# Optimization experiments

Measured on AMD Instinct MI355X. Metric: run time of the kernel, lower is better.

## Reference

```python
import jax, jax.numpy as jnp
import numpy as np

B, S, D = 4, 2048, 2048
NH, NKV = 16, 4
HD = D // NH            # 128
DKV = NKV * HD          # 512
REP = NH // NKV         # 4
SCALE = HD ** -0.5
EPS = 1e-9


def setup_inputs() -> dict:
    key = jax.random.key(0)
    ks = jax.random.split(key, 9)
    s = 0.02
    return {
        "q": jax.random.normal(ks[0], (B, S, D), jnp.float32),
        "k": jax.random.normal(ks[1], (B, S, D), jnp.float32),
        "v": jax.random.normal(ks[2], (B, S, D), jnp.float32),
        "Wq": jax.random.normal(ks[3], (D, D), jnp.float32) * s,
        "bq": jnp.zeros((D,), jnp.float32),
        "Wk": jax.random.normal(ks[4], (D, DKV), jnp.float32) * s,
        "bk": jnp.zeros((DKV,), jnp.float32),
        "Wv": jax.random.normal(ks[5], (D, DKV), jnp.float32) * s,
        "bv": jnp.zeros((DKV,), jnp.float32),
    }


def reference(q, k, v, Wq, bq, Wk, bk, Wv, bv):
    # Dense projections (nn.Dense = x @ W + b)
    qh = q @ Wq + bq                      # (B, S, D)
    kh = k @ Wk + bk                      # (B, S, DKV)
    vh = v @ Wv + bv                      # (B, S, DKV)
    # Faithful to source: repeat along axis=-2 (the SEQUENCE axis)
    kh = jnp.repeat(kh, REP, axis=-2)     # (B, S*REP, DKV)
    vh = jnp.repeat(vh, REP, axis=-2)     # (B, S*REP, DKV)
    # flash_attention math: reshape to (B, S, NH, HD) -> (B, NH, S, HD)
    qh = qh.reshape(B, S, NH, HD).transpose(0, 2, 1, 3)
    kh = kh.reshape(B, S, NH, HD).transpose(0, 2, 1, 3)
    vh = vh.reshape(B, S, NH, HD).transpose(0, 2, 1, 3)
    attn = jnp.einsum("bhqd,bhkd->bhqk", qh, kh) * SCALE
    m = jnp.max(attn, axis=-1, keepdims=True)
    e = jnp.exp(attn - m)
    p = e / (jnp.sum(e, axis=-1, keepdims=True) + EPS)
    out = jnp.einsum("bhqk,bhkd->bhqd", p, vh)   # (B, NH, S, HD)
    return out.transpose(0, 2, 1, 3).reshape(B, S, D)
```

## Files before the change

kernel.cpp:

```cpp
#include <hip/hip_runtime.h>

#define B_    4
#define S_    2048
#define D_    2048
#define NH_   16
#define NKV_  4
#define HD_   128
#define DKV_  512
#define QSCALE_ ((float)(0.08838834764831845 * 1.4426950408889634))

typedef __attribute__((ext_vector_type(8))) short          bf16x8;
typedef __attribute__((ext_vector_type(8))) unsigned short us8;
typedef __attribute__((ext_vector_type(4))) unsigned short us4;
typedef __attribute__((ext_vector_type(4))) float          f32x4;

__device__ __forceinline__ unsigned short f2bf(float f) {
    union { float f; unsigned int u; } v; v.f = f;
    unsigned int u = v.u;
    u += 0x7fffu + ((u >> 16) & 1u);
    return (unsigned short)(u >> 16);
}

__device__ __forceinline__ unsigned int cvt_pk_bf16(float lo, float hi) {
    unsigned int r;
    asm volatile("v_cvt_pk_bf16_f32 %0, %1, %2" : "=v"(r) : "v"(lo), "v"(hi));
    return r;
}

__device__ __forceinline__ float vmax3(float a, float b, float c) {
    float r;
    asm("v_max3_f32 %0, %1, %2, %3" : "=v"(r) : "v"(a), "v"(b), "v"(c));
    return r;
}

#define GLOAD16(gp, lp) __builtin_amdgcn_global_load_lds(                      \
    (const __attribute__((address_space(1))) unsigned int*)(gp),              \
    (__attribute__((address_space(3))) unsigned int*)(lp), 16, 0, 0)

__device__ __forceinline__ void tr_body(
    const float* __restrict__ W, unsigned short* __restrict__ WT,
    int K, int N, int kb, int nb, float (*tile)[33])
{
    const int k0 = kb * 32, n0 = nb * 32;
    const int tx = threadIdx.x & 31, ty = threadIdx.x >> 5;
#pragma unroll
    for (int i = 0; i < 32; i += 8)
        tile[ty + i][tx] = W[(size_t)(k0 + ty + i) * N + n0 + tx];
    __syncthreads();
#pragma unroll
    for (int i = 0; i < 32; i += 8)
        WT[(size_t)(n0 + ty + i) * K + k0 + tx] = f2bf(tile[tx][ty + i]);
}

__global__ __launch_bounds__(256) void transpose_all(
    const float* __restrict__ Wq, const float* __restrict__ Wk,
    const float* __restrict__ Wv, unsigned short* __restrict__ WqT,
    unsigned short* __restrict__ WkT, unsigned short* __restrict__ WvT)
{
    __shared__ float tile[32][33];
    const int y = blockIdx.y;
    if (y < 64)       tr_body(Wq, WqT, D_, D_,   blockIdx.x, y,      tile);
    else if (y < 80)  tr_body(Wk, WkT, D_, DKV_, blockIdx.x, y - 64, tile);
    else              tr_body(Wv, WvT, D_, DKV_, blockIdx.x, y - 80, tile);
}

__device__ __forceinline__ void cvt_body(
    const float* __restrict__ src, unsigned short* __restrict__ dst, int n8)
{
    int i = blockIdx.x * blockDim.x + threadIdx.x;
    const int stride = gridDim.x * blockDim.x;
    const float4* p = (const float4*)src;
    us8* o8 = (us8*)dst;
    for (; i < n8; i += stride) {
        float4 a = p[2 * i], b = p[2 * i + 1];
        us8 o;
        o[0] = f2bf(a.x); o[1] = f2bf(a.y); o[2] = f2bf(a.z); o[3] = f2bf(a.w);
        o[4] = f2bf(b.x); o[5] = f2bf(b.y); o[6] = f2bf(b.z); o[7] = f2bf(b.w);
        o8[i] = o;
    }
}

__global__ __launch_bounds__(256) void cvt_bf16(
    const float* __restrict__ in, unsigned short* __restrict__ out, int n8)
{
    cvt_body(in, out, n8);
}

__global__ __launch_bounds__(256) void cvt_all(
    const float* __restrict__ q, const float* __restrict__ k,
    const float* __restrict__ v, unsigned short* __restrict__ xq,
    unsigned short* __restrict__ xk, unsigned short* __restrict__ xv)
{
    const int which = blockIdx.y;
    const float* src = which == 0 ? q : which == 1 ? k : v;
    unsigned short* dst = which == 0 ? xq : which == 1 ? xk : xv;
    cvt_body(src, dst, B_ * S_ * D_ / 8);
}

__device__ __forceinline__ void gemm_body(
    const unsigned short* __restrict__ A, const unsigned short* __restrict__ BT,
    const float* __restrict__ bias, unsigned short* __restrict__ C,
    int N, int nb, float scale, int vmode,
    unsigned short* As , unsigned short* Bs )
{
    const int K = D_;
    const int m0 = blockIdx.x * 128, n0 = nb * 128;
    const int t = threadIdx.x;
    const int w = t >> 6, l = t & 63, lr = l & 15, lg = l >> 4;
    const int wr = (w >> 1) * 64, wc = (w & 1) * 64;
    const int sr = t >> 2, sc = (t & 3) * 8;

    const unsigned short* aS = A + (size_t)(m0 + sr) * K + sc;
    const unsigned short* bS = BT + (size_t)(n0 + sr) * K + sc;

    auto stage = [&](int buf, int kt) {
        GLOAD16(aS + kt * 32,                    &As[buf * 4096 + t * 8]);
        GLOAD16(aS + (size_t)64 * K + kt * 32,   &As[buf * 4096 + 2048 + t * 8]);
        GLOAD16(bS + kt * 32,                    &Bs[buf * 4096 + t * 8]);
        GLOAD16(bS + (size_t)64 * K + kt * 32,   &Bs[buf * 4096 + 2048 + t * 8]);
    };

    f32x4 acc[4][4] = {};
    stage(0, 0);
    __syncthreads();

    const int nk = K / 32;
    int cur = 0;
    for (int kt = 0; kt < nk; ++kt) {
        if (kt + 1 < nk) stage(cur ^ 1, kt + 1);

        bf16x8 af[4], bfv[4];
#pragma unroll
        for (int i = 0; i < 4; ++i)
            af[i] = *(const bf16x8*)&As[cur * 4096 + (wr + i * 16 + lr) * 32 + lg * 8];
#pragma unroll
        for (int i = 0; i < 4; ++i)
            bfv[i] = *(const bf16x8*)&Bs[cur * 4096 + (wc + i * 16 + lr) * 32 + lg * 8];
#pragma unroll
        for (int i = 0; i < 4; ++i)
#pragma unroll
            for (int j = 0; j < 4; ++j)
                acc[i][j] = __builtin_amdgcn_mfma_f32_16x16x32_bf16(
                    af[i], bfv[j], acc[i][j], 0, 0, 0);

        __syncthreads();
        cur ^= 1;
    }

#pragma unroll
    for (int j = 0; j < 4; ++j) {
        const int col = n0 + wc + j * 16 + lr;
        const float bv = bias[col];
#pragma unroll
        for (int i = 0; i < 4; ++i) {
            const int row0 = m0 + wr + i * 16 + lg * 4;
            if (vmode == 0) {
#pragma unroll
                for (int r = 0; r < 4; ++r)
                    C[(size_t)(row0 + r) * N + col] = f2bf((acc[i][j][r] + bv) * scale);
            } else {
                const int bb = row0 >> 11, s0 = row0 & (S_ - 1);
                us4 hv;
#pragma unroll
                for (int r = 0; r < 4; ++r) hv[r] = f2bf((acc[i][j][r] + bv) * scale);
                *(us4*)&C[((size_t)bb * N + col) * S_ + s0] = hv;
            }
        }
    }
}

__global__ __launch_bounds__(256) void gemm_all(
    const unsigned short* __restrict__ xq, const unsigned short* __restrict__ xk,
    const unsigned short* __restrict__ xv,
    const unsigned short* __restrict__ WqT, const unsigned short* __restrict__ WkT,
    const unsigned short* __restrict__ WvT,
    const float* __restrict__ bq, const float* __restrict__ bk,
    const float* __restrict__ bv,
    unsigned short* __restrict__ qh, unsigned short* __restrict__ kh,
    unsigned short* __restrict__ vhT)
{
    __shared__ __align__(16) unsigned short As[2 * 128 * 32];
    __shared__ __align__(16) unsigned short Bs[2 * 128 * 32];
    const int y = blockIdx.y;
    if (y < 16)      gemm_body(xq, WqT, bq, qh,  D_,   y,      QSCALE_, 0, As, Bs);
    else if (y < 20) gemm_body(xk, WkT, bk, kh,  DKV_, y - 16, 1.0f,    0, As, Bs);
    else             gemm_body(xv, WvT, bv, vhT, DKV_, y - 20, 1.0f,    1, As, Bs);
}

__global__ __launch_bounds__(256) void gemm_lds(
    const unsigned short* __restrict__ A, const unsigned short* __restrict__ BT,
    const float* __restrict__ bias, unsigned short* __restrict__ C,
    int N, float scale, int vmode)
{
    __shared__ __align__(16) unsigned short As[2 * 128 * 32];
    __shared__ __align__(16) unsigned short Bs[2 * 128 * 32];
    gemm_body(A, BT, bias, C, N, blockIdx.y, scale, vmode, As, Bs);
}

template <int VMODE>
__global__ __launch_bounds__(256) void gemm_rs(
    const float* __restrict__ A, const unsigned short* __restrict__ BT,
    const float* __restrict__ bias, unsigned short* __restrict__ C,
    int M, int N, int K, float scale)
{
    __shared__ unsigned short As[128][40];
    __shared__ unsigned short Bs[128][40];

    const int m0 = blockIdx.x * 128, n0 = blockIdx.y * 128;
    const int t = threadIdx.x;
    const int sr = t >> 1, sc = (t & 1) * 16;
    const int w = t >> 6, l = t & 63, lr = l & 15, lg = l >> 4;
    const int wr = (w >> 1) * 64, wc = (w & 1) * 64;

    const float* aptr = A + (size_t)(m0 + sr) * K + sc;
    const unsigned short* bptr = BT + (size_t)(n0 + sr) * K + sc;

    float4 pa0, pa1, pa2, pa3;
    us8 pb0, pb1;
    auto prefetch = [&](int k0) {
        const float4* ap = (const float4*)(aptr + k0);
        pa0 = ap[0]; pa1 = ap[1]; pa2 = ap[2]; pa3 = ap[3];
        const us8* bp = (const us8*)(bptr + k0);
        pb0 = bp[0]; pb1 = bp[1];
    };

    f32x4 acc[4][4] = {};
    prefetch(0);
    const int nk = K / 32;
    for (int kt = 0; kt < nk; ++kt) {
        __syncthreads();
        us8 c0, c1;
        c0[0] = f2bf(pa0.x); c0[1] = f2bf(pa0.y); c0[2] = f2bf(pa0.z); c0[3] = f2bf(pa0.w);
        c0[4] = f2bf(pa1.x); c0[5] = f2bf(pa1.y); c0[6] = f2bf(pa1.z); c0[7] = f2bf(pa1.w);
        c1[0] = f2bf(pa2.x); c1[1] = f2bf(pa2.y); c1[2] = f2bf(pa2.z); c1[3] = f2bf(pa2.w);
        c1[4] = f2bf(pa3.x); c1[5] = f2bf(pa3.y); c1[6] = f2bf(pa3.z); c1[7] = f2bf(pa3.w);
        *(us8*)&As[sr][sc]     = c0;
        *(us8*)&As[sr][sc + 8] = c1;
        *(us8*)&Bs[sr][sc]     = pb0;
        *(us8*)&Bs[sr][sc + 8] = pb1;
        __syncthreads();
        if (kt + 1 < nk) prefetch((kt + 1) * 32);

        bf16x8 af[4], bfv[4];
#pragma unroll
        for (int i = 0; i < 4; ++i)
            af[i] = *(const bf16x8*)&As[wr + i * 16 + lr][lg * 8];
#pragma unroll
        for (int i = 0; i < 4; ++i)
            bfv[i] = *(const bf16x8*)&Bs[wc + i * 16 + lr][lg * 8];
#pragma unroll
        for (int i = 0; i < 4; ++i)
#pragma unroll
            for (int j = 0; j < 4; ++j)
                acc[i][j] = __builtin_amdgcn_mfma_f32_16x16x32_bf16(
                    af[i], bfv[j], acc[i][j], 0, 0, 0);
    }

#pragma unroll
    for (int j = 0; j < 4; ++j) {
        const int col = n0 + wc + j * 16 + lr;
        const float bv = bias[col];
#pragma unroll
        for (int i = 0; i < 4; ++i) {
            const int row0 = m0 + wr + i * 16 + lg * 4;
            if (VMODE == 0) {
#pragma unroll
                for (int r = 0; r < 4; ++r)
                    C[(size_t)(row0 + r) * N + col] = f2bf((acc[i][j][r] + bv) * scale);
            } else {
                const int bb = row0 >> 11, s0 = row0 & (S_ - 1);
                us4 hv;
#pragma unroll
                for (int r = 0; r < 4; ++r) hv[r] = f2bf((acc[i][j][r] + bv) * scale);
                *(us4*)&C[((size_t)bb * N + col) * S_ + s0] = hv;
            }
        }
    }
}

__global__ __launch_bounds__(256, 2) void attn_kernel(
    const unsigned short* __restrict__ qh, const unsigned short* __restrict__ kh,
    const unsigned short* __restrict__ vhT, float* __restrict__ out)
{
    __shared__ __align__(16) unsigned short Kd[2][64 * 128];
    __shared__ __align__(16) unsigned short Vd[2][128 * 64];
    __shared__ __align__(16) unsigned int   P2T[4][16 * 44];

    const int qb = blockIdx.x, h = blockIdx.y, b = blockIdx.z;
    const int g = h & (NKV_ - 1);
    const int t = threadIdx.x, w = t >> 6, l = t & 63, lr = l & 15, lg = l >> 4;
    const int q0 = qb * 128 + w * 32;

    bf16x8 qf[2][4];
#pragma unroll
    for (int rf = 0; rf < 2; ++rf) {
        const unsigned short* qrow =
            qh + ((size_t)(b * S_) + q0 + rf * 16 + lr) * D_ + h * HD_;
#pragma unroll
        for (int ko = 0; ko < 4; ++ko)
            qf[rf][ko] = *(const bf16x8*)(qrow + ko * 32 + lg * 8);
    }

    bf16x8 onesf;
#pragma unroll
    for (int j = 0; j < 8; ++j) onesf[j] = (short)0x3F80;

    f32x4 o[2][8] = {};
    f32x4 oe[2] = {};
    float mrow[2] = {-1e30f, -1e30f};

    const unsigned short* kb_ = kh + (size_t)b * S_ * DKV_ + g * HD_;
    const unsigned short* vb_ = vhT + ((size_t)b * DKV_ + g * HD_) * S_;

    const int kc = ((t & 15) * 8) ^ (((t >> 4) & 7) << 3);
    const int vc = ((t & 7) * 8) ^ (((t >> 3) & 7) << 3);

    auto stage = [&](int buf, int kt) {
        const unsigned short* ks = kb_ + (size_t)(kt * 64) * DKV_ + kc;
        const unsigned short* vs = vb_ + kt * 64 + vc;
#pragma unroll
        for (int i = 0; i < 4; ++i)
            GLOAD16(ks + (size_t)(i * 16 + (t >> 4)) * DKV_, &Kd[buf][i * 2048 + t * 8]);
#pragma unroll
        for (int i = 0; i < 4; ++i)
            GLOAD16(vs + (size_t)(i * 32 + (t >> 3)) * S_,   &Vd[buf][i * 2048 + t * 8]);
    };

    stage(0, 0);
    stage(1, 1);

    const int swz = (lr & 7) << 3;
    unsigned int* pw = &P2T[w][lr * 44];
    int cur = 0;
    const int NT = S_ / 64;
    for (int kt = 0; kt < NT; ++kt) {
        if (kt + 1 < NT) { asm volatile("s_waitcnt vmcnt(8)" ::: "memory"); }
        else             { asm volatile("s_waitcnt vmcnt(0)" ::: "memory"); }
        __builtin_amdgcn_s_barrier();
        __builtin_amdgcn_sched_barrier(0);

        f32x4 sa[2][4] = {};
        __builtin_amdgcn_s_setprio(1);
#pragma unroll
        for (int cf = 0; cf < 4; ++cf)
#pragma unroll
            for (int ko = 0; ko < 4; ++ko) {
                bf16x8 kf = *(const bf16x8*)
                    &Kd[cur][(cf * 16 + lr) * 128 + ((ko * 32 + lg * 8) ^ swz)];
                sa[0][cf] = __builtin_amdgcn_mfma_f32_16x16x32_bf16(kf, qf[0][ko], sa[0][cf], 0, 0, 0);
                sa[1][cf] = __builtin_amdgcn_mfma_f32_16x16x32_bf16(kf, qf[1][ko], sa[1][cf], 0, 0, 0);
            }
        __builtin_amdgcn_s_setprio(0);

        bf16x8 pa[2][2];
#pragma unroll
        for (int rf = 0; rf < 2; ++rf) {
            const float m0v = vmax3(sa[rf][0][0], sa[rf][0][1], sa[rf][0][2]);
            const float m1v = vmax3(sa[rf][0][3], sa[rf][1][0], sa[rf][1][1]);
            const float m2v = vmax3(sa[rf][1][2], sa[rf][1][3], sa[rf][2][0]);
            const float m3v = vmax3(sa[rf][2][1], sa[rf][2][2], sa[rf][2][3]);
            const float m4v = vmax3(sa[rf][3][0], sa[rf][3][1], sa[rf][3][2]);
            const float mxl = fmaxf(vmax3(m0v, m1v, m2v),
                                    vmax3(m3v, m4v, sa[rf][3][3]));
            float m = mrow[rf];
            if (!__all(mxl <= m + 8.f)) {
                float mx = fmaxf(mxl, m);
                mx = fmaxf(mx, __shfl_xor(mx, 16));
                mx = fmaxf(mx, __shfl_xor(mx, 32));
                const float al = exp2f(m - mx);
                mrow[rf] = m = mx;
#pragma unroll
                for (int r = 0; r < 4; ++r) {
                    const float a = __shfl(al, lg * 4 + r);
                    oe[rf][r] *= a;
#pragma unroll
                    for (int df = 0; df < 8; ++df) o[rf][df][r] *= a;
                }
            }
            float p[4][4];
#pragma unroll
            for (int cf = 0; cf < 4; ++cf)
#pragma unroll
                for (int r = 0; r < 4; ++r)
                    p[cf][r] = exp2f(sa[rf][cf][r] - m);
#pragma unroll
            for (int cf = 0; cf < 4; ++cf) {
                uint2 pk;
                pk.x = cvt_pk_bf16(p[cf][0], p[cf][1]);
                pk.y = cvt_pk_bf16(p[cf][2], p[cf][3]);
                *(uint2*)&pw[cf * 8 + lg * 2] = pk;
            }
            pa[rf][0] = *(const bf16x8*)&pw[lg * 4];
            pa[rf][1] = *(const bf16x8*)&pw[16 + lg * 4];
        }

        __builtin_amdgcn_s_setprio(1);
#pragma unroll
        for (int ks = 0; ks < 2; ++ks)
#pragma unroll
            for (int df = 0; df < 8; ++df) {
                bf16x8 vf = *(const bf16x8*)
                    &Vd[cur][(df * 16 + lr) * 64 + ((ks * 32 + lg * 8) ^ swz)];
                o[0][df] = __builtin_amdgcn_mfma_f32_16x16x32_bf16(pa[0][ks], vf, o[0][df], 0, 0, 0);
                o[1][df] = __builtin_amdgcn_mfma_f32_16x16x32_bf16(pa[1][ks], vf, o[1][df], 0, 0, 0);
            }
        oe[0] = __builtin_amdgcn_mfma_f32_16x16x32_bf16(pa[0][0], onesf, oe[0], 0, 0, 0);
        oe[0] = __builtin_amdgcn_mfma_f32_16x16x32_bf16(pa[0][1], onesf, oe[0], 0, 0, 0);
        oe[1] = __builtin_amdgcn_mfma_f32_16x16x32_bf16(pa[1][0], onesf, oe[1], 0, 0, 0);
        oe[1] = __builtin_amdgcn_mfma_f32_16x16x32_bf16(pa[1][1], onesf, oe[1], 0, 0, 0);
        __builtin_amdgcn_s_setprio(0);

        __builtin_amdgcn_sched_barrier(0);
        __builtin_amdgcn_s_barrier();
        __builtin_amdgcn_sched_barrier(0);
        if (kt + 2 < NT) stage(cur, kt + 2);
        cur ^= 1;
    }

#pragma unroll
    for (int rf = 0; rf < 2; ++rf) {
        float* ob = out + ((size_t)(b * S_) + q0 + rf * 16 + lg * 4) * D_ + h * HD_;
#pragma unroll
        for (int r = 0; r < 4; ++r) {
            const float inv = 1.f / (oe[rf][r] + 1e-9f);
#pragma unroll
            for (int df = 0; df < 8; ++df)
                ob[(size_t)r * D_ + df * 16 + lr] = o[rf][df][r] * inv;
        }
    }
}

extern "C" void kernel_launch(void* const* d_in, const int* in_sizes, int n_in,
                              void* d_out, int out_size, void* d_ws, size_t ws_size,
                              hipStream_t stream)
{
    const float* q  = (const float*)d_in[0];
    const float* k  = (const float*)d_in[1];
    const float* v  = (const float*)d_in[2];
    const float* Wq = (const float*)d_in[3];
    const float* bq = (const float*)d_in[4];
    const float* Wk = (const float*)d_in[5];
    const float* bk = (const float*)d_in[6];
    const float* Wv = (const float*)d_in[7];
    const float* bv = (const float*)d_in[8];
    float* out = (float*)d_out;

    char* ws = (char*)d_ws;
    unsigned short* qh  = (unsigned short*)ws; ws += (size_t)B_ * S_ * D_ * 2;
    unsigned short* kh  = (unsigned short*)ws; ws += (size_t)B_ * S_ * DKV_ * 2;
    unsigned short* vhT = (unsigned short*)ws; ws += (size_t)B_ * DKV_ * S_ * 2;
    unsigned short* WqT = (unsigned short*)ws; ws += (size_t)D_ * D_ * 2;
    unsigned short* WkT = (unsigned short*)ws; ws += (size_t)DKV_ * D_ * 2;
    unsigned short* WvT = (unsigned short*)ws; ws += (size_t)DKV_ * D_ * 2;
    unsigned short* xq  = (unsigned short*)ws; ws += (size_t)B_ * S_ * D_ * 2;
    unsigned short* xk  = (unsigned short*)ws; ws += (size_t)B_ * S_ * D_ * 2;
    unsigned short* xv  = (unsigned short*)ws; ws += (size_t)B_ * S_ * D_ * 2;

    const size_t need3 = (size_t)163577856;
    const size_t need1 = (size_t)96468992;

    transpose_all<<<dim3(64, 96), 256, 0, stream>>>(Wq, Wk, Wv, WqT, WkT, WvT);

    const int M = B_ * S_;
    const int n8 = M * D_ / 8;

    if (ws_size >= need3) {
        cvt_all<<<dim3(1024, 3), 256, 0, stream>>>(q, k, v, xq, xk, xv);
        gemm_all<<<dim3(M / 128, 24), 256, 0, stream>>>(
            xq, xk, xv, WqT, WkT, WvT, bq, bk, bv, qh, kh, vhT);
    } else if (ws_size >= need1) {
        cvt_bf16<<<2048, 256, 0, stream>>>(q, xq, n8);
        gemm_lds<<<dim3(M / 128, D_ / 128), 256, 0, stream>>>(xq, WqT, bq, qh, D_, QSCALE_, 0);
        cvt_bf16<<<2048, 256, 0, stream>>>(k, xq, n8);
        gemm_lds<<<dim3(M / 128, DKV_ / 128), 256, 0, stream>>>(xq, WkT, bk, kh, DKV_, 1.0f, 0);
        cvt_bf16<<<2048, 256, 0, stream>>>(v, xq, n8);
        gemm_lds<<<dim3(M / 128, DKV_ / 128), 256, 0, stream>>>(xq, WvT, bv, vhT, DKV_, 1.0f, 1);
    } else {
        gemm_rs<0><<<dim3(M / 128, D_ / 128), 256, 0, stream>>>(q, WqT, bq, qh, M, D_, D_, QSCALE_);
        gemm_rs<0><<<dim3(M / 128, DKV_ / 128), 256, 0, stream>>>(k, WkT, bk, kh, M, DKV_, D_, 1.0f);
        gemm_rs<1><<<dim3(M / 128, DKV_ / 128), 256, 0, stream>>>(v, WvT, bv, vhT, M, DKV_, D_, 1.0f);
    }

    attn_kernel<<<dim3(S_ / 128, NH_, B_), 256, 0, stream>>>(qh, kh, vhT, out);
}
```

Before: 395.6 us.

## Single-buffer V tile, shuffle P in registers, and raise attention occupancy

Removes the per-wave LDS P transpose buffer and instead builds the P operand for the PV MFMA with cross-lane shuffles, permuting the V read offsets to match the new k-ordering. V is now single-buffered and loaded one tile ahead, with an extra wait and barrier before the PV stage, and launch bounds rise from 2 to 3 blocks per SIMD. The lower LDS use is meant to allow higher occupancy and to drop the LDS round trip for P. In exchange there is an extra barrier per iteration and less prefetch distance for V, which may expose load latency.

```diff
diff --git a/kernel.cpp b/kernel.cpp
--- a/kernel.cpp
+++ b/kernel.cpp
@@ -31,6 +31,13 @@
     float r;
     asm("v_max3_f32 %0, %1, %2, %3" : "=v"(r) : "v"(a), "v"(b), "v"(c));
     return r;
+}
+
+__device__ __forceinline__ bf16x8 pack4(unsigned int a, unsigned int b,
+                                        unsigned int c, unsigned int d) {
+    union { unsigned int u[4]; bf16x8 v; } x;
+    x.u[0] = a; x.u[1] = b; x.u[2] = c; x.u[3] = d;
+    return x.v;
 }
 
 #define GLOAD16(gp, lp) __builtin_amdgcn_global_load_lds(                      \
@@ -278,18 +285,19 @@
     }
 }
 
-__global__ __launch_bounds__(256, 2) void attn_kernel(
+__global__ __launch_bounds__(256, 3) void attn_kernel(
     const unsigned short* __restrict__ qh, const unsigned short* __restrict__ kh,
     const unsigned short* __restrict__ vhT, float* __restrict__ out)
 {
     __shared__ __align__(16) unsigned short Kd[2][64 * 128];
-    __shared__ __align__(16) unsigned short Vd[2][128 * 64];
-    __shared__ __align__(16) unsigned int   P2T[4][16 * 44];
+    __shared__ __align__(16) unsigned short Vd[128 * 64];
 
     const int qb = blockIdx.x, h = blockIdx.y, b = blockIdx.z;
     const int g = h & (NKV_ - 1);
     const int t = threadIdx.x, w = t >> 6, l = t & 63, lr = l & 15, lg = l >> 4;
     const int q0 = qb * 128 + w * 32;
+    const bool godd = (lg & 1) != 0;
+    const int sU8 = ((((lg & 1) ^ 1) << 1) + (lg >> 1)) * 8;
 
     bf16x8 qf[2][4];
 #pragma unroll
@@ -315,27 +323,29 @@
     const int kc = ((t & 15) * 8) ^ (((t >> 4) & 7) << 3);
     const int vc = ((t & 7) * 8) ^ (((t >> 3) & 7) << 3);
 
-    auto stage = [&](int buf, int kt) {
+    auto stageK = [&](int buf, int kt) {
         const unsigned short* ks = kb_ + (size_t)(kt * 64) * DKV_ + kc;
+#pragma unroll
+        for (int i = 0; i < 4; ++i)
+            GLOAD16(ks + (size_t)(i * 16 + (t >> 4)) * DKV_, &Kd[buf][i * 2048 + t * 8]);
+    };
+    auto stageV = [&](int kt) {
         const unsigned short* vs = vb_ + kt * 64 + vc;
 #pragma unroll
         for (int i = 0; i < 4; ++i)
-            GLOAD16(ks + (size_t)(i * 16 + (t >> 4)) * DKV_, &Kd[buf][i * 2048 + t * 8]);
-#pragma unroll
-        for (int i = 0; i < 4; ++i)
-            GLOAD16(vs + (size_t)(i * 32 + (t >> 3)) * S_,   &Vd[buf][i * 2048 + t * 8]);
+            GLOAD16(vs + (size_t)(i * 32 + (t >> 3)) * S_, &Vd[i * 2048 + t * 8]);
     };
 
-    stage(0, 0);
-    stage(1, 1);
+    stageK(0, 0);
+    stageV(0);
+    stageK(1, 1);
 
     const int swz = (lr & 7) << 3;
-    unsigned int* pw = &P2T[w][lr * 44];
     int cur = 0;
     const int NT = S_ / 64;
     for (int kt = 0; kt < NT; ++kt) {
         if (kt + 1 < NT) { asm volatile("s_waitcnt vmcnt(8)" ::: "memory"); }
-        else             { asm volatile("s_waitcnt vmcnt(0)" ::: "memory"); }
+        else             { asm volatile("s_waitcnt vmcnt(4)" ::: "memory"); }
         __builtin_amdgcn_s_barrier();
         __builtin_amdgcn_sched_barrier(0);
 
@@ -383,27 +393,43 @@
 #pragma unroll
                 for (int r = 0; r < 4; ++r)
                     p[cf][r] = exp2f(sa[rf][cf][r] - m);
+            unsigned int xp[4][2];
 #pragma unroll
             for (int cf = 0; cf < 4; ++cf) {
-                uint2 pk;
-                pk.x = cvt_pk_bf16(p[cf][0], p[cf][1]);
-                pk.y = cvt_pk_bf16(p[cf][2], p[cf][3]);
-                *(uint2*)&pw[cf * 8 + lg * 2] = pk;
+                xp[cf][0] = cvt_pk_bf16(p[cf][0], p[cf][1]);
+                xp[cf][1] = cvt_pk_bf16(p[cf][2], p[cf][3]);
             }
-            pa[rf][0] = *(const bf16x8*)&pw[lg * 4];
-            pa[rf][1] = *(const bf16x8*)&pw[16 + lg * 4];
+#pragma unroll
+            for (int pi = 0; pi < 2; ++pi) {
+                const int c0 = pi * 2, c1 = c0 + 1;
+                const int t0 = __shfl_xor((int)xp[c0][0], 16);
+                const int u0 = __shfl_xor((int)xp[c1][0], 16);
+                const int t1 = __shfl_xor((int)xp[c0][1], 16);
+                const int u1 = __shfl_xor((int)xp[c1][1], 16);
+                const unsigned int e0 = godd ? (unsigned int)t0 : xp[c1][0];
+                const unsigned int e1 = godd ? (unsigned int)t1 : xp[c1][1];
+                const unsigned int o0 = godd ? xp[c0][0] : (unsigned int)u0;
+                const unsigned int o1 = godd ? xp[c0][1] : (unsigned int)u1;
+                pa[rf][pi] = pack4(e0, e1, o0, o1);
+            }
         }
 
+        if (kt + 1 < NT) { asm volatile("s_waitcnt vmcnt(4)" ::: "memory"); }
+        else             { asm volatile("s_waitcnt vmcnt(0)" ::: "memory"); }
+        __builtin_amdgcn_s_barrier();
+        __builtin_amdgcn_sched_barrier(0);
+
         __builtin_amdgcn_s_setprio(1);
 #pragma unroll
-        for (int ks = 0; ks < 2; ++ks)
-#pragma unroll
-            for (int df = 0; df < 8; ++df) {
-                bf16x8 vf = *(const bf16x8*)
-                    &Vd[cur][(df * 16 + lr) * 64 + ((ks * 32 + lg * 8) ^ swz)];
-                o[0][df] = __builtin_amdgcn_mfma_f32_16x16x32_bf16(pa[0][ks], vf, o[0][df], 0, 0, 0);
-                o[1][df] = __builtin_amdgcn_mfma_f32_16x16x32_bf16(pa[1][ks], vf, o[1][df], 0, 0, 0);
-            }
+        for (int df = 0; df < 8; ++df) {
+            const int rbase = (df * 16 + lr) * 64;
+            bf16x8 vfU = *(const bf16x8*)&Vd[rbase + (sU8 ^ swz)];
+            bf16x8 vfW = *(const bf16x8*)&Vd[rbase + ((sU8 + 32) ^ swz)];
+            o[0][df] = __builtin_amdgcn_mfma_f32_16x16x32_bf16(pa[0][0], vfU, o[0][df], 0, 0, 0);
+            o[1][df] = __builtin_amdgcn_mfma_f32_16x16x32_bf16(pa[1][0], vfU, o[1][df], 0, 0, 0);
+            o[0][df] = __builtin_amdgcn_mfma_f32_16x16x32_bf16(pa[0][1], vfW, o[0][df], 0, 0, 0);
+            o[1][df] = __builtin_amdgcn_mfma_f32_16x16x32_bf16(pa[1][1], vfW, o[1][df], 0, 0, 0);
+        }
         oe[0] = __builtin_amdgcn_mfma_f32_16x16x32_bf16(pa[0][0], onesf, oe[0], 0, 0, 0);
         oe[0] = __builtin_amdgcn_mfma_f32_16x16x32_bf16(pa[0][1], onesf, oe[0], 0, 0, 0);
         oe[1] = __builtin_amdgcn_mfma_f32_16x16x32_bf16(pa[1][0], onesf, oe[1], 0, 0, 0);
@@ -413,7 +439,8 @@
         __builtin_amdgcn_sched_barrier(0);
         __builtin_amdgcn_s_barrier();
         __builtin_amdgcn_sched_barrier(0);
-        if (kt + 2 < NT) stage(cur, kt + 2);
+        if (kt + 1 < NT) stageV(kt + 1);
+        if (kt + 2 < NT) stageK(cur, kt + 2);
         cur ^= 1;
     }
 
```

After: 410.9 us. 1.04x slower.

## Enlarge attention query tile, shrink KV tile, keep P in registers

Applied to the files above, without the earlier changes.

Each wave now handles 64 query rows instead of 32 (256 per block), and each K/V tile holds 32 keys instead of 64, which halves LDS footprint and doubles reuse of each staged K/V fragment. The 16x16x32 MFMA output layout for a 32-key tile matches the A-operand layout, so the P matrix is packed directly into registers and the LDS round-trip for P is removed. V is read from LDS as two 4-element halves with a new swizzle. Register pressure rises sharply (o grows to 4x8 accumulators), and the grid halves to 512 blocks, which risks lower occupancy and spills.

```diff
diff --git a/kernel.cpp b/kernel.cpp
--- a/kernel.cpp
+++ b/kernel.cpp
@@ -10,6 +10,7 @@
 #define QSCALE_ ((float)(0.08838834764831845 * 1.4426950408889634))
 
 typedef __attribute__((ext_vector_type(8))) short          bf16x8;
+typedef __attribute__((ext_vector_type(4))) short          bf16x4;
 typedef __attribute__((ext_vector_type(8))) unsigned short us8;
 typedef __attribute__((ext_vector_type(4))) unsigned short us4;
 typedef __attribute__((ext_vector_type(4))) float          f32x4;
@@ -31,6 +32,13 @@
     float r;
     asm("v_max3_f32 %0, %1, %2, %3" : "=v"(r) : "v"(a), "v"(b), "v"(c));
     return r;
+}
+
+__device__ __forceinline__ bf16x8 pack4(unsigned int a, unsigned int b,
+                                        unsigned int c, unsigned int d) {
+    union { unsigned int u[4]; bf16x8 v; } x;
+    x.u[0] = a; x.u[1] = b; x.u[2] = c; x.u[3] = d;
+    return x.v;
 }
 
 #define GLOAD16(gp, lp) __builtin_amdgcn_global_load_lds(                      \
@@ -282,18 +290,17 @@
     const unsigned short* __restrict__ qh, const unsigned short* __restrict__ kh,
     const unsigned short* __restrict__ vhT, float* __restrict__ out)
 {
-    __shared__ __align__(16) unsigned short Kd[2][64 * 128];
-    __shared__ __align__(16) unsigned short Vd[2][128 * 64];
-    __shared__ __align__(16) unsigned int   P2T[4][16 * 44];
+    __shared__ __align__(16) unsigned short Kd[2][32 * 128];
+    __shared__ __align__(16) unsigned short Vd[2][128 * 32];
 
     const int qb = blockIdx.x, h = blockIdx.y, b = blockIdx.z;
     const int g = h & (NKV_ - 1);
     const int t = threadIdx.x, w = t >> 6, l = t & 63, lr = l & 15, lg = l >> 4;
-    const int q0 = qb * 128 + w * 32;
-
-    bf16x8 qf[2][4];
-#pragma unroll
-    for (int rf = 0; rf < 2; ++rf) {
+    const int q0 = qb * 256 + w * 64;
+
+    bf16x8 qf[4][4];
+#pragma unroll
+    for (int rf = 0; rf < 4; ++rf) {
         const unsigned short* qrow =
             qh + ((size_t)(b * S_) + q0 + rf * 16 + lr) * D_ + h * HD_;
 #pragma unroll
@@ -305,63 +312,69 @@
 #pragma unroll
     for (int j = 0; j < 8; ++j) onesf[j] = (short)0x3F80;
 
-    f32x4 o[2][8] = {};
-    f32x4 oe[2] = {};
-    float mrow[2] = {-1e30f, -1e30f};
+    f32x4 o[4][8] = {};
+    f32x4 oe[4] = {};
+    float mrow[4];
+#pragma unroll
+    for (int rf = 0; rf < 4; ++rf) mrow[rf] = -1e30f;
 
     const unsigned short* kb_ = kh + (size_t)b * S_ * DKV_ + g * HD_;
     const unsigned short* vb_ = vhT + ((size_t)b * DKV_ + g * HD_) * S_;
 
-    const int kc = ((t & 15) * 8) ^ (((t >> 4) & 7) << 3);
-    const int vc = ((t & 7) * 8) ^ (((t >> 3) & 7) << 3);
-
     auto stage = [&](int buf, int kt) {
-        const unsigned short* ks = kb_ + (size_t)(kt * 64) * DKV_ + kc;
-        const unsigned short* vs = vb_ + kt * 64 + vc;
-#pragma unroll
-        for (int i = 0; i < 4; ++i)
-            GLOAD16(ks + (size_t)(i * 16 + (t >> 4)) * DKV_, &Kd[buf][i * 2048 + t * 8]);
-#pragma unroll
-        for (int i = 0; i < 4; ++i)
-            GLOAD16(vs + (size_t)(i * 32 + (t >> 3)) * S_,   &Vd[buf][i * 2048 + t * 8]);
+#pragma unroll
+        for (int i = 0; i < 2; ++i) {
+            const int ch = i * 256 + t;
+            const int r = ch >> 4, c = ch & 15;
+            const int lc = (c & 8) | ((c & 7) ^ (r & 7));
+            GLOAD16(kb_ + (size_t)(kt * 32 + r) * DKV_ + lc * 8,
+                    &Kd[buf][ch * 8]);
+        }
+#pragma unroll
+        for (int i = 0; i < 2; ++i) {
+            const int ch = i * 256 + t;
+            const int d = ch >> 2, c = ch & 3;
+            const int L = (2 * c) ^ (d & 6);
+            GLOAD16(vb_ + (size_t)d * S_ + kt * 32 + L * 4,
+                    &Vd[buf][ch * 8]);
+        }
     };
 
     stage(0, 0);
     stage(1, 1);
 
     const int swz = (lr & 7) << 3;
-    unsigned int* pw = &P2T[w][lr * 44];
+    const int ua = lg ^ (lr & 6);
     int cur = 0;
-    const int NT = S_ / 64;
+    const int NT = S_ / 32;
     for (int kt = 0; kt < NT; ++kt) {
-        if (kt + 1 < NT) { asm volatile("s_waitcnt vmcnt(8)" ::: "memory"); }
+        if (kt + 1 < NT) { asm volatile("s_waitcnt vmcnt(4)" ::: "memory"); }
         else             { asm volatile("s_waitcnt vmcnt(0)" ::: "memory"); }
         __builtin_amdgcn_s_barrier();
         __builtin_amdgcn_sched_barrier(0);
 
-        f32x4 sa[2][4] = {};
+        f32x4 sa[4][2] = {};
         __builtin_amdgcn_s_setprio(1);
 #pragma unroll
-        for (int cf = 0; cf < 4; ++cf)
+        for (int cf = 0; cf < 2; ++cf)
 #pragma unroll
             for (int ko = 0; ko < 4; ++ko) {
                 bf16x8 kf = *(const bf16x8*)
                     &Kd[cur][(cf * 16 + lr) * 128 + ((ko * 32 + lg * 8) ^ swz)];
                 sa[0][cf] = __builtin_amdgcn_mfma_f32_16x16x32_bf16(kf, qf[0][ko], sa[0][cf], 0, 0, 0);
                 sa[1][cf] = __builtin_amdgcn_mfma_f32_16x16x32_bf16(kf, qf[1][ko], sa[1][cf], 0, 0, 0);
+                sa[2][cf] = __builtin_amdgcn_mfma_f32_16x16x32_bf16(kf, qf[2][ko], sa[2][cf], 0, 0, 0);
+                sa[3][cf] = __builtin_amdgcn_mfma_f32_16x16x32_bf16(kf, qf[3][ko], sa[3][cf], 0, 0, 0);
             }
         __builtin_amdgcn_s_setprio(0);
 
-        bf16x8 pa[2][2];
-#pragma unroll
-        for (int rf = 0; rf < 2; ++rf) {
-            const float m0v = vmax3(sa[rf][0][0], sa[rf][0][1], sa[rf][0][2]);
-            const float m1v = vmax3(sa[rf][0][3], sa[rf][1][0], sa[rf][1][1]);
-            const float m2v = vmax3(sa[rf][1][2], sa[rf][1][3], sa[rf][2][0]);
-            const float m3v = vmax3(sa[rf][2][1], sa[rf][2][2], sa[rf][2][3]);
-            const float m4v = vmax3(sa[rf][3][0], sa[rf][3][1], sa[rf][3][2]);
-            const float mxl = fmaxf(vmax3(m0v, m1v, m2v),
-                                    vmax3(m3v, m4v, sa[rf][3][3]));
+        bf16x8 pa[4];
+#pragma unroll
+        for (int rf = 0; rf < 4; ++rf) {
+            const float mxl =
+                fmaxf(vmax3(sa[rf][0][0], sa[rf][0][1], sa[rf][0][2]),
+                      vmax3(sa[rf][0][3], sa[rf][1][0],
+                            vmax3(sa[rf][1][1], sa[rf][1][2], sa[rf][1][3])));
             float m = mrow[rf];
             if (!__all(mxl <= m + 8.f)) {
                 float mx = fmaxf(mxl, m);
@@ -377,37 +390,34 @@
                     for (int df = 0; df < 8; ++df) o[rf][df][r] *= a;
                 }
             }
-            float p[4][4];
-#pragma unroll
-            for (int cf = 0; cf < 4; ++cf)
+            float p[2][4];
+#pragma unroll
+            for (int cf = 0; cf < 2; ++cf)
 #pragma unroll
                 for (int r = 0; r < 4; ++r)
                     p[cf][r] = exp2f(sa[rf][cf][r] - m);
-#pragma unroll
-            for (int cf = 0; cf < 4; ++cf) {
-                uint2 pk;
-                pk.x = cvt_pk_bf16(p[cf][0], p[cf][1]);
-                pk.y = cvt_pk_bf16(p[cf][2], p[cf][3]);
-                *(uint2*)&pw[cf * 8 + lg * 2] = pk;
-            }
-            pa[rf][0] = *(const bf16x8*)&pw[lg * 4];
-            pa[rf][1] = *(const bf16x8*)&pw[16 + lg * 4];
+            pa[rf] = pack4(cvt_pk_bf16(p[0][0], p[0][1]),
+                           cvt_pk_bf16(p[0][2], p[0][3]),
+                           cvt_pk_bf16(p[1][0], p[1][1]),
+                           cvt_pk_bf16(p[1][2], p[1][3]));
         }
 
         __builtin_amdgcn_s_setprio(1);
 #pragma unroll
-        for (int ks = 0; ks < 2; ++ks)
-#pragma unroll
-            for (int df = 0; df < 8; ++df) {
-                bf16x8 vf = *(const bf16x8*)
-                    &Vd[cur][(df * 16 + lr) * 64 + ((ks * 32 + lg * 8) ^ swz)];
-                o[0][df] = __builtin_amdgcn_mfma_f32_16x16x32_bf16(pa[0][ks], vf, o[0][df], 0, 0, 0);
-                o[1][df] = __builtin_amdgcn_mfma_f32_16x16x32_bf16(pa[1][ks], vf, o[1][df], 0, 0, 0);
-            }
-        oe[0] = __builtin_amdgcn_mfma_f32_16x16x32_bf16(pa[0][0], onesf, oe[0], 0, 0, 0);
-        oe[0] = __builtin_amdgcn_mfma_f32_16x16x32_bf16(pa[0][1], onesf, oe[0], 0, 0, 0);
-        oe[1] = __builtin_amdgcn_mfma_f32_16x16x32_bf16(pa[1][0], onesf, oe[1], 0, 0, 0);
-        oe[1] = __builtin_amdgcn_mfma_f32_16x16x32_bf16(pa[1][1], onesf, oe[1], 0, 0, 0);
+        for (int df = 0; df < 8; ++df) {
+            const int rb = (df * 16 + lr) * 32;
+            bf16x4 va  = *(const bf16x4*)&Vd[cur][rb + ua * 4];
+            bf16x4 vb2 = *(const bf16x4*)&Vd[cur][rb + (ua ^ 4) * 4];
+            bf16x8 vf = __builtin_shufflevector(va, vb2, 0, 1, 2, 3, 4, 5, 6, 7);
+            o[0][df] = __builtin_amdgcn_mfma_f32_16x16x32_bf16(pa[0], vf, o[0][df], 0, 0, 0);
+            o[1][df] = __builtin_amdgcn_mfma_f32_16x16x32_bf16(pa[1], vf, o[1][df], 0, 0, 0);
+            o[2][df] = __builtin_amdgcn_mfma_f32_16x16x32_bf16(pa[2], vf, o[2][df], 0, 0, 0);
+            o[3][df] = __builtin_amdgcn_mfma_f32_16x16x32_bf16(pa[3], vf, o[3][df], 0, 0, 0);
+        }
+        oe[0] = __builtin_amdgcn_mfma_f32_16x16x32_bf16(pa[0], onesf, oe[0], 0, 0, 0);
+        oe[1] = __builtin_amdgcn_mfma_f32_16x16x32_bf16(pa[1], onesf, oe[1], 0, 0, 0);
+        oe[2] = __builtin_amdgcn_mfma_f32_16x16x32_bf16(pa[2], onesf, oe[2], 0, 0, 0);
+        oe[3] = __builtin_amdgcn_mfma_f32_16x16x32_bf16(pa[3], onesf, oe[3], 0, 0, 0);
         __builtin_amdgcn_s_setprio(0);
 
         __builtin_amdgcn_sched_barrier(0);
@@ -418,7 +428,7 @@
     }
 
 #pragma unroll
-    for (int rf = 0; rf < 2; ++rf) {
+    for (int rf = 0; rf < 4; ++rf) {
         float* ob = out + ((size_t)(b * S_) + q0 + rf * 16 + lg * 4) * D_ + h * HD_;
 #pragma unroll
         for (int r = 0; r < 4; ++r) {
@@ -481,5 +491,5 @@
         gemm_rs<1><<<dim3(M / 128, DKV_ / 128), 256, 0, stream>>>(v, WvT, bv, vhT, M, DKV_, D_, 1.0f);
     }
 
-    attn_kernel<<<dim3(S_ / 128, NH_, B_), 256, 0, stream>>>(qh, kh, vhT, out);
-}
+    attn_kernel<<<dim3(S_ / 256, NH_, B_), 256, 0, stream>>>(qh, kh, vhT, out);
+}
```

Result: slower. 422.4 us (+6.8%).
